# Kernel tuning notes

Measured on AMD Instinct MI355X. Metric: run time of the kernel, lower is better.

## Reference

```python
import jax, jax.numpy as jnp
import numpy as np
import math

HIDDEN = 1024
HEADS = 16
HEAD_DIM = HIDDEN // HEADS
B, S = 2, 2048


def setup_inputs() -> dict:
    key = jax.random.key(0)
    ks = jax.random.split(key, 10)
    std = 1.0 / math.sqrt(HIDDEN)
    mk = lambda k: (jax.random.normal(k, (HIDDEN, HIDDEN), jnp.float32) * std)
    return {
        "hidden_states": jax.random.normal(ks[0], (B, S, HIDDEN), jnp.float32),
        "attention_mask": jnp.zeros((B, 1, 1, S), jnp.float32),
        "wq": mk(ks[1]), "bq": jnp.zeros((HIDDEN,), jnp.float32),
        "wk": mk(ks[2]), "bk": jnp.zeros((HIDDEN,), jnp.float32),
        "wv": mk(ks[3]), "bv": jnp.zeros((HIDDEN,), jnp.float32),
        "wo": mk(ks[4]), "bo": jnp.zeros((HIDDEN,), jnp.float32),
    }


def reference(hidden_states, attention_mask, wq, bq, wk, bk, wv, bv, wo, bo):
    b, s, _ = hidden_states.shape
    scale = math.sqrt(HEAD_DIM)
    # projections (torch Linear: x @ W.T + b); weights stored as [out, in]
    q = hidden_states @ wq.T + bq
    k = hidden_states @ wk.T + bk
    v = hidden_states @ wv.T + bv
    # [B, H, S, D]
    q = q.reshape(b, s, HEADS, HEAD_DIM).transpose(0, 2, 1, 3)
    k = k.reshape(b, s, HEADS, HEAD_DIM).transpose(0, 2, 1, 3)
    v = v.reshape(b, s, HEADS, HEAD_DIM).transpose(0, 2, 1, 3)
    scores = jnp.einsum("bhqd,bhkd->bhqk", q, k) / scale
    scores = scores + attention_mask  # broadcast [B,1,1,S]
    weights = jax.nn.softmax(scores, axis=-1)  # dropout = identity (eval)
    out = jnp.einsum("bhqk,bhkd->bhqd", weights, v)
    out = out.transpose(0, 2, 1, 3).reshape(b, s, HIDDEN)
    out = out @ wo.T + bo
    return out
```

## Files before the change

kernel.cpp:

```cpp
#include <hip/hip_runtime.h>
#include <hip/hip_bf16.h>

typedef __bf16 bf16_t;
typedef __bf16 bf16x8 __attribute__((ext_vector_type(8)));
typedef float f32x4 __attribute__((ext_vector_type(4)));

#define SEQ    2048
#define NH     16
#define HD     64
#define HIDDEN 1024
#define PSTR   72
#define LOG2E  1.44269504f

__device__ __forceinline__ bf16_t to_bf16(float f) { return (bf16_t)f; }

__device__ __forceinline__ void async16(const bf16_t* g, bf16_t* l) {
    __builtin_amdgcn_global_load_lds((const __attribute__((address_space(1))) void*)g,
                                     (__attribute__((address_space(3))) void*)l, 16, 0, 0);
}

__global__ __launch_bounds__(256) void cvt_kernel(
    const float* __restrict__ s0, bf16_t* __restrict__ d0, int c0,
    const float* __restrict__ s1, bf16_t* __restrict__ d1, int c1,
    const float* __restrict__ s2, bf16_t* __restrict__ d2, int c2,
    const float* __restrict__ s3, bf16_t* __restrict__ d3, int c3)
{
    int blk = blockIdx.x;
    const float* s; bf16_t* d;
    if (blk < c0)              { s = s0; d = d0; }
    else if ((blk -= c0) < c1) { s = s1; d = d1; }
    else if ((blk -= c1) < c2) { s = s2; d = d2; }
    else                       { blk -= c2; s = s3; d = d3; }
    const size_t base = (size_t)blk * 2048 + threadIdx.x * 8;
    const float4 a = *(const float4*)&s[base];
    const float4 b = *(const float4*)&s[base + 4];
    bf16x8 o;
    o[0] = (bf16_t)a.x; o[1] = (bf16_t)a.y; o[2] = (bf16_t)a.z; o[3] = (bf16_t)a.w;
    o[4] = (bf16_t)b.x; o[5] = (bf16_t)b.y; o[6] = (bf16_t)b.z; o[7] = (bf16_t)b.w;
    *(bf16x8*)&d[base] = o;
}

__global__ __launch_bounds__(256, 3) void qkv_kernel(
    const bf16_t* __restrict__ X,
    const bf16_t* __restrict__ wq, const bf16_t* __restrict__ wk, const bf16_t* __restrict__ wv,
    const float* __restrict__ bq, const float* __restrict__ bk, const float* __restrict__ bv,
    bf16_t* __restrict__ qws, bf16_t* __restrict__ kws, bf16_t* __restrict__ vws)
{
    __shared__ __align__(16) bf16_t As[128 * 64];
    __shared__ __align__(16) bf16_t Bs[128 * 64];
    const int z = blockIdx.z;
    const bf16_t* Wsel = (z == 0) ? wq : (z == 1) ? wk : wv;
    const float*  bsel = (z == 0) ? bq : (z == 1) ? bk : bv;
    bf16_t* dst        = (z == 0) ? qws : (z == 1) ? kws : vws;
    const int m0 = blockIdx.y * 128, n0 = blockIdx.x * 128;

    const int t = threadIdx.x, lane = t & 63, w = t >> 6;
    const int w0 = w & 1, w1 = w >> 1, l15 = lane & 15, q4 = lane >> 4;

    f32x4 acc[4][4];
#pragma unroll
    for (int i = 0; i < 4; i++)
#pragma unroll
        for (int j = 0; j < 4; j++) acc[i][j] = f32x4{0.f, 0.f, 0.f, 0.f};

    for (int kt = 0; kt < HIDDEN; kt += 64) {
#pragma unroll
        for (int j = 0; j < 4; j++) {
            const int s = j * 256 + t;
            const int row = s >> 3, c = (s & 7) ^ (row & 7);
            const int lbase = (j * 256 + w * 64) * 8;
            async16(&X[(size_t)(m0 + row) * HIDDEN + kt + c * 8], &As[lbase]);
            async16(&Wsel[(size_t)(n0 + row) * HIDDEN + kt + c * 8], &Bs[lbase]);
        }
        __syncthreads();
#pragma unroll
        for (int ks = 0; ks < 2; ks++) {
            bf16x8 af[4];
#pragma unroll
            for (int ti = 0; ti < 4; ti++) {
                const int ra = w0 * 64 + ti * 16 + l15;
                af[ti] = *(const bf16x8*)&As[ra * 64 + (((ks * 4 + q4) ^ (ra & 7))) * 8];
            }
#pragma unroll
            for (int tj = 0; tj < 4; tj++) {
                const int rb = w1 * 64 + tj * 16 + l15;
                const bf16x8 bfr = *(const bf16x8*)&Bs[rb * 64 + (((ks * 4 + q4) ^ (rb & 7))) * 8];
#pragma unroll
                for (int ti = 0; ti < 4; ti++)
                    acc[ti][tj] = __builtin_amdgcn_mfma_f32_16x16x32_bf16(af[ti], bfr, acc[ti][tj], 0, 0, 0);
            }
        }
        __syncthreads();
    }

#pragma unroll
    for (int tj = 0; tj < 4; tj++) {
        const int n = n0 + w1 * 64 + tj * 16 + l15;
        const float bb = bsel[n];
        const int hh = n >> 6, d = n & 63;
#pragma unroll
        for (int ti = 0; ti < 4; ti++)
#pragma unroll
            for (int r = 0; r < 4; r++) {
                const int m = m0 + w0 * 64 + ti * 16 + q4 * 4 + r;
                const float val = acc[ti][tj][r] + bb;
                if (z < 2) {
                    dst[(size_t)m * HIDDEN + n] = to_bf16(val);
                } else {
                    const int b = m >> 11, s = m & (SEQ - 1);
                    dst[(((size_t)b * NH + hh) * HD + d) * SEQ + s] = to_bf16(val);
                }
            }
    }
}

__global__ __launch_bounds__(256, 2) void attn_kernel(
    const bf16_t* __restrict__ Qw, const bf16_t* __restrict__ Kw,
    const bf16_t* __restrict__ Vtw, const float* __restrict__ Mask,
    bf16_t* __restrict__ Ow)
{
    __shared__ __align__(16) bf16_t Ks[64 * 64];
    __shared__ __align__(16) bf16_t Vs[64 * 64];
    __shared__ __align__(16) bf16_t Ps[4 * 32 * PSTR];

    const int t = threadIdx.x, lane = t & 63, w = t >> 6;
    const int l15 = lane & 15, q4 = lane >> 4;
    const int lid = blockIdx.x + 16 * blockIdx.y;
    const int c8 = lid & 7, j = lid >> 3;
    const int bh = (c8 << 2) | (j >> 4);
    const int q0 = (j & 15) << 7;
    const int b = bh >> 4, h = bh & 15;

    const bf16_t* Qh = Qw + (size_t)b * SEQ * HIDDEN + h * HD;
    const bf16_t* Kh = Kw + (size_t)b * SEQ * HIDDEN + h * HD;
    const bf16_t* Vh = Vtw + (size_t)bh * HD * SEQ;
    const float* Mrow = Mask + (size_t)b * SEQ;

    bf16x8 qf[2][2];
#pragma unroll
    for (int rb = 0; rb < 2; rb++)
#pragma unroll
        for (int ks = 0; ks < 2; ks++)
            qf[rb][ks] = *(const bf16x8*)&Qh[(size_t)(q0 + w * 32 + rb * 16 + l15) * HIDDEN + ks * 32 + q4 * 8];

    f32x4 oacc[2][4];
#pragma unroll
    for (int rb = 0; rb < 2; rb++)
#pragma unroll
        for (int nb = 0; nb < 4; nb++) oacc[rb][nb] = f32x4{0.f, 0.f, 0.f, 0.f};
    float psum[2][4] = {{0.f, 0.f, 0.f, 0.f}, {0.f, 0.f, 0.f, 0.f}};

    for (int kt = 0; kt < SEQ; kt += 64) {
#pragma unroll
        for (int jj = 0; jj < 2; jj++) {
            const int s = jj * 256 + t;
            const int row = s >> 3, c = (s & 7) ^ (row & 7);
            const int lbase = (jj * 256 + w * 64) * 8;
            async16(&Kh[(size_t)(kt + row) * HIDDEN + c * 8], &Ks[lbase]);
            async16(&Vh[(size_t)row * SEQ + kt + c * 8], &Vs[lbase]);
        }
        __syncthreads();

        f32x4 sa[2][4];
#pragma unroll
        for (int rb = 0; rb < 2; rb++)
#pragma unroll
            for (int cb = 0; cb < 4; cb++) sa[rb][cb] = f32x4{0.f, 0.f, 0.f, 0.f};
#pragma unroll
        for (int cb = 0; cb < 4; cb++)
#pragma unroll
            for (int ks = 0; ks < 2; ks++) {
                const int r = cb * 16 + l15;
                const bf16x8 kf = *(const bf16x8*)&Ks[r * 64 + (((ks * 4 + q4) ^ (r & 7))) * 8];
                sa[0][cb] = __builtin_amdgcn_mfma_f32_16x16x32_bf16(qf[0][ks], kf, sa[0][cb], 0, 0, 0);
                sa[1][cb] = __builtin_amdgcn_mfma_f32_16x16x32_bf16(qf[1][ks], kf, sa[1][cb], 0, 0, 0);
            }

#pragma unroll
        for (int cb = 0; cb < 4; cb++) {
            const float mk2 = Mrow[kt + cb * 16 + l15] * LOG2E;
#pragma unroll
            for (int rb = 0; rb < 2; rb++)
#pragma unroll
                for (int r = 0; r < 4; r++) {
                    const float p = exp2f(fmaf(sa[rb][cb][r], 0.125f * LOG2E, mk2));
                    psum[rb][r] += p;
                    Ps[(w * 32 + rb * 16 + q4 * 4 + r) * PSTR + cb * 16 + l15] = to_bf16(p);
                }
        }

#pragma unroll
        for (int ks = 0; ks < 2; ks++) {
            const bf16x8 pf0 = *(const bf16x8*)&Ps[(w * 32 +      l15) * PSTR + ks * 32 + q4 * 8];
            const bf16x8 pf1 = *(const bf16x8*)&Ps[(w * 32 + 16 + l15) * PSTR + ks * 32 + q4 * 8];
#pragma unroll
            for (int nb = 0; nb < 4; nb++) {
                const int rv = nb * 16 + l15;
                const bf16x8 vf = *(const bf16x8*)&Vs[rv * 64 + (((ks * 4 + q4) ^ (rv & 7))) * 8];
                oacc[0][nb] = __builtin_amdgcn_mfma_f32_16x16x32_bf16(pf0, vf, oacc[0][nb], 0, 0, 0);
                oacc[1][nb] = __builtin_amdgcn_mfma_f32_16x16x32_bf16(pf1, vf, oacc[1][nb], 0, 0, 0);
            }
        }
        __syncthreads();
    }

#pragma unroll
    for (int rb = 0; rb < 2; rb++)
#pragma unroll
        for (int r = 0; r < 4; r++) {
#pragma unroll
            for (int off = 1; off < 16; off <<= 1) psum[rb][r] += __shfl_xor(psum[rb][r], off);
        }
#pragma unroll
    for (int rb = 0; rb < 2; rb++)
#pragma unroll
        for (int r = 0; r < 4; r++) {
            const float inv = 1.f / psum[rb][r];
            const int s = q0 + w * 32 + rb * 16 + q4 * 4 + r;
#pragma unroll
            for (int nb = 0; nb < 4; nb++) {
                const int d = nb * 16 + l15;
                Ow[((size_t)b * SEQ + s) * HIDDEN + h * HD + d] = to_bf16(oacc[rb][nb][r] * inv);
            }
        }
}

__global__ __launch_bounds__(256, 2) void oproj_kernel(
    const bf16_t* __restrict__ A, const bf16_t* __restrict__ Wo,
    const float* __restrict__ bo, float* __restrict__ Out)
{
    __shared__ __align__(16) bf16_t As[64 * 64];
    __shared__ __align__(16) bf16_t Bs[128 * 64];
    const int m0 = blockIdx.y * 64, n0 = blockIdx.x * 128;
    const int t = threadIdx.x, lane = t & 63, w = t >> 6;
    const int l15 = lane & 15, q4 = lane >> 4;

    f32x4 acc[4][2];
#pragma unroll
    for (int i = 0; i < 4; i++)
#pragma unroll
        for (int j = 0; j < 2; j++) acc[i][j] = f32x4{0.f, 0.f, 0.f, 0.f};

    for (int kt = 0; kt < HIDDEN; kt += 64) {
#pragma unroll
        for (int j = 0; j < 2; j++) {
            const int s = j * 256 + t;
            const int row = s >> 3, c = (s & 7) ^ (row & 7);
            async16(&A[(size_t)(m0 + row) * HIDDEN + kt + c * 8], &As[(j * 256 + w * 64) * 8]);
        }
#pragma unroll
        for (int j = 0; j < 4; j++) {
            const int s = j * 256 + t;
            const int row = s >> 3, c = (s & 7) ^ (row & 7);
            async16(&Wo[(size_t)(n0 + row) * HIDDEN + kt + c * 8], &Bs[(j * 256 + w * 64) * 8]);
        }
        __syncthreads();
#pragma unroll
        for (int ks = 0; ks < 2; ks++) {
            bf16x8 af[4];
#pragma unroll
            for (int ti = 0; ti < 4; ti++) {
                const int ra = ti * 16 + l15;
                af[ti] = *(const bf16x8*)&As[ra * 64 + (((ks * 4 + q4) ^ (ra & 7))) * 8];
            }
#pragma unroll
            for (int tj = 0; tj < 2; tj++) {
                const int rb = w * 32 + tj * 16 + l15;
                const bf16x8 bfr = *(const bf16x8*)&Bs[rb * 64 + (((ks * 4 + q4) ^ (rb & 7))) * 8];
#pragma unroll
                for (int ti = 0; ti < 4; ti++)
                    acc[ti][tj] = __builtin_amdgcn_mfma_f32_16x16x32_bf16(af[ti], bfr, acc[ti][tj], 0, 0, 0);
            }
        }
        __syncthreads();
    }

#pragma unroll
    for (int tj = 0; tj < 2; tj++) {
        const int n = n0 + w * 32 + tj * 16 + l15;
        const float bb = bo[n];
#pragma unroll
        for (int ti = 0; ti < 4; ti++)
#pragma unroll
            for (int r = 0; r < 4; r++) {
                const int m = m0 + ti * 16 + q4 * 4 + r;
                Out[(size_t)m * HIDDEN + n] = acc[ti][tj][r] + bb;
            }
    }
}

extern "C" void kernel_launch(void* const* d_in, const int* in_sizes, int n_in,
                              void* d_out, int out_size, void* d_ws, size_t ws_size,
                              hipStream_t stream) {
    const float* X   = (const float*)d_in[0];
    const float* msk = (const float*)d_in[1];
    const float* wq  = (const float*)d_in[2];
    const float* bq  = (const float*)d_in[3];
    const float* wk  = (const float*)d_in[4];
    const float* bk  = (const float*)d_in[5];
    const float* wv  = (const float*)d_in[6];
    const float* bv  = (const float*)d_in[7];
    const float* wo  = (const float*)d_in[8];
    const float* bo  = (const float*)d_in[9];
    float* out = (float*)d_out;

    const size_t NELT = (size_t)2 * SEQ * HIDDEN;
    const size_t WELT = (size_t)HIDDEN * HIDDEN;
    bf16_t* xbf = (bf16_t*)d_ws;
    bf16_t* qws = xbf + NELT;
    bf16_t* kws = qws + NELT;
    bf16_t* vws = kws + NELT;
    bf16_t* aws = xbf;
    bf16_t* wqb = (bf16_t*)d_out;
    bf16_t* wkb = wqb + WELT;
    bf16_t* wvb = wkb + WELT;
    bf16_t* wob = qws;

    cvt_kernel<<<dim3(2048 + 3 * 512), dim3(256), 0, stream>>>(
        X, xbf, 2048, wq, wqb, 512, wk, wkb, 512, wv, wvb, 512);
    qkv_kernel<<<dim3(8, 32, 3), dim3(256), 0, stream>>>(
        xbf, wqb, wkb, wvb, bq, bk, bv, qws, kws, vws);
    attn_kernel<<<dim3(16, 32), dim3(256), 0, stream>>>(qws, kws, vws, msk, aws);
    cvt_kernel<<<dim3(512), dim3(256), 0, stream>>>(
        wo, wob, 512, wo, wob, 0, wo, wob, 0, wo, wob, 0);
    oproj_kernel<<<dim3(8, 64), dim3(256), 0, stream>>>(aws, wob, bo, out);
}
```

Baseline: 229.5 us.

## Keep P in registers via transposed QK MFMA and split keys across warps

The attention kernel computes S^T (K as the A operand) so each lane already holds P in the layout needed for the PV MFMA. P is fed straight from registers as fp16 into 16x16x16 f16 MFMAs, which removes the shared-memory round trip for P. To support this, V is stored as fp16. Query tiles shrink to 64 rows, and the two warp pairs each process half of the key sequence. Their partial outputs and row sums are combined through LDS at the end. This doubles the grid to 1024 blocks and raises the occupancy hint to 4, at the cost of an extra reduction step and fp16 range limits on unnormalized probabilities.

```diff
diff --git a/kernel.cpp b/kernel.cpp
--- a/kernel.cpp
+++ b/kernel.cpp
@@ -3,18 +3,18 @@
 
 typedef __bf16 bf16_t;
 typedef __bf16 bf16x8 __attribute__((ext_vector_type(8)));
+typedef _Float16 f16x4 __attribute__((ext_vector_type(4)));
 typedef float f32x4 __attribute__((ext_vector_type(4)));
 
 #define SEQ    2048
 #define NH     16
 #define HD     64
 #define HIDDEN 1024
-#define PSTR   72
 #define LOG2E  1.44269504f
 
 __device__ __forceinline__ bf16_t to_bf16(float f) { return (bf16_t)f; }
 
-__device__ __forceinline__ void async16(const bf16_t* g, bf16_t* l) {
+__device__ __forceinline__ void async16(const void* g, void* l) {
     __builtin_amdgcn_global_load_lds((const __attribute__((address_space(1))) void*)g,
                                      (__attribute__((address_space(3))) void*)l, 16, 0, 0);
 }
@@ -44,14 +44,13 @@
     const bf16_t* __restrict__ X,
     const bf16_t* __restrict__ wq, const bf16_t* __restrict__ wk, const bf16_t* __restrict__ wv,
     const float* __restrict__ bq, const float* __restrict__ bk, const float* __restrict__ bv,
-    bf16_t* __restrict__ qws, bf16_t* __restrict__ kws, bf16_t* __restrict__ vws)
+    bf16_t* __restrict__ qws, bf16_t* __restrict__ kws, _Float16* __restrict__ vws)
 {
     __shared__ __align__(16) bf16_t As[128 * 64];
     __shared__ __align__(16) bf16_t Bs[128 * 64];
     const int z = blockIdx.z;
     const bf16_t* Wsel = (z == 0) ? wq : (z == 1) ? wk : wv;
     const float*  bsel = (z == 0) ? bq : (z == 1) ? bk : bv;
-    bf16_t* dst        = (z == 0) ? qws : (z == 1) ? kws : vws;
     const int m0 = blockIdx.y * 128, n0 = blockIdx.x * 128;
 
     const int t = threadIdx.x, lane = t & 63, w = t >> 6;
@@ -104,125 +103,153 @@
             for (int r = 0; r < 4; r++) {
                 const int m = m0 + w0 * 64 + ti * 16 + q4 * 4 + r;
                 const float val = acc[ti][tj][r] + bb;
-                if (z < 2) {
-                    dst[(size_t)m * HIDDEN + n] = to_bf16(val);
-                } else {
+                if (z == 0)      qws[(size_t)m * HIDDEN + n] = to_bf16(val);
+                else if (z == 1) kws[(size_t)m * HIDDEN + n] = to_bf16(val);
+                else {
                     const int b = m >> 11, s = m & (SEQ - 1);
-                    dst[(((size_t)b * NH + hh) * HD + d) * SEQ + s] = to_bf16(val);
+                    vws[(((size_t)b * NH + hh) * HD + d) * SEQ + s] = (_Float16)val;
                 }
             }
     }
 }
 
-__global__ __launch_bounds__(256, 2) void attn_kernel(
+__global__ __launch_bounds__(256, 4) void attn_kernel(
     const bf16_t* __restrict__ Qw, const bf16_t* __restrict__ Kw,
-    const bf16_t* __restrict__ Vtw, const float* __restrict__ Mask,
+    const _Float16* __restrict__ Vtw, const float* __restrict__ Mask,
     bf16_t* __restrict__ Ow)
 {
-    __shared__ __align__(16) bf16_t Ks[64 * 64];
-    __shared__ __align__(16) bf16_t Vs[64 * 64];
-    __shared__ __align__(16) bf16_t Ps[4 * 32 * PSTR];
+    __shared__ __align__(16) bf16_t Tiles[2][2][64 * 64];
 
     const int t = threadIdx.x, lane = t & 63, w = t >> 6;
     const int l15 = lane & 15, q4 = lane >> 4;
-    const int lid = blockIdx.x + 16 * blockIdx.y;
+    const int wq = w & 1, kh = w >> 1;
+    const int lid = blockIdx.x;
     const int c8 = lid & 7, j = lid >> 3;
-    const int bh = (c8 << 2) | (j >> 4);
-    const int q0 = (j & 15) << 7;
+    const int bh = c8 * 4 + (j >> 5);
+    const int q0 = (j & 31) * 64;
     const int b = bh >> 4, h = bh & 15;
 
     const bf16_t* Qh = Qw + (size_t)b * SEQ * HIDDEN + h * HD;
     const bf16_t* Kh = Kw + (size_t)b * SEQ * HIDDEN + h * HD;
-    const bf16_t* Vh = Vtw + (size_t)bh * HD * SEQ;
+    const _Float16* Vh = Vtw + (size_t)bh * HD * SEQ;
     const float* Mrow = Mask + (size_t)b * SEQ;
 
     bf16x8 qf[2][2];
 #pragma unroll
-    for (int rb = 0; rb < 2; rb++)
+    for (int nq = 0; nq < 2; nq++)
 #pragma unroll
         for (int ks = 0; ks < 2; ks++)
-            qf[rb][ks] = *(const bf16x8*)&Qh[(size_t)(q0 + w * 32 + rb * 16 + l15) * HIDDEN + ks * 32 + q4 * 8];
+            qf[nq][ks] = *(const bf16x8*)&Qh[(size_t)(q0 + wq * 32 + nq * 16 + l15) * HIDDEN + ks * 32 + q4 * 8];
 
     f32x4 oacc[2][4];
 #pragma unroll
-    for (int rb = 0; rb < 2; rb++)
-#pragma unroll
-        for (int nb = 0; nb < 4; nb++) oacc[rb][nb] = f32x4{0.f, 0.f, 0.f, 0.f};
-    float psum[2][4] = {{0.f, 0.f, 0.f, 0.f}, {0.f, 0.f, 0.f, 0.f}};
-
-    for (int kt = 0; kt < SEQ; kt += 64) {
-#pragma unroll
-        for (int jj = 0; jj < 2; jj++) {
-            const int s = jj * 256 + t;
+    for (int nq = 0; nq < 2; nq++)
+#pragma unroll
+        for (int nb = 0; nb < 4; nb++) oacc[nq][nb] = f32x4{0.f, 0.f, 0.f, 0.f};
+    float psum[2] = {0.f, 0.f};
+
+    bf16_t* Ksh = &Tiles[kh][0][0];
+    _Float16* Vsh = (_Float16*)&Tiles[kh][1][0];
+    const int kbase = kh * (SEQ / 2);
+
+    for (int it = 0; it < 16; it++) {
+        const int kt = kbase + it * 64;
+#pragma unroll
+        for (int jj = 0; jj < 4; jj++) {
+            const int s = jj * 128 + wq * 64 + lane;
             const int row = s >> 3, c = (s & 7) ^ (row & 7);
-            const int lbase = (jj * 256 + w * 64) * 8;
-            async16(&Kh[(size_t)(kt + row) * HIDDEN + c * 8], &Ks[lbase]);
-            async16(&Vh[(size_t)row * SEQ + kt + c * 8], &Vs[lbase]);
+            const int lbase = (jj * 128 + wq * 64) * 8;
+            async16(&Kh[(size_t)(kt + row) * HIDDEN + c * 8], &Ksh[lbase]);
+            async16(&Vh[(size_t)row * SEQ + kt + c * 8], &Vsh[lbase]);
         }
         __syncthreads();
 
         f32x4 sa[2][4];
 #pragma unroll
-        for (int rb = 0; rb < 2; rb++)
-#pragma unroll
-            for (int cb = 0; cb < 4; cb++) sa[rb][cb] = f32x4{0.f, 0.f, 0.f, 0.f};
+        for (int nq = 0; nq < 2; nq++)
+#pragma unroll
+            for (int cb = 0; cb < 4; cb++) sa[nq][cb] = f32x4{0.f, 0.f, 0.f, 0.f};
 #pragma unroll
         for (int cb = 0; cb < 4; cb++)
 #pragma unroll
             for (int ks = 0; ks < 2; ks++) {
-                const int r = cb * 16 + l15;
-                const bf16x8 kf = *(const bf16x8*)&Ks[r * 64 + (((ks * 4 + q4) ^ (r & 7))) * 8];
-                sa[0][cb] = __builtin_amdgcn_mfma_f32_16x16x32_bf16(qf[0][ks], kf, sa[0][cb], 0, 0, 0);
-                sa[1][cb] = __builtin_amdgcn_mfma_f32_16x16x32_bf16(qf[1][ks], kf, sa[1][cb], 0, 0, 0);
-            }
-
+                const int rk = cb * 16 + l15;
+                const bf16x8 kf = *(const bf16x8*)&Ksh[rk * 64 + (((ks * 4 + q4) ^ (rk & 7))) * 8];
+                sa[0][cb] = __builtin_amdgcn_mfma_f32_16x16x32_bf16(kf, qf[0][ks], sa[0][cb], 0, 0, 0);
+                sa[1][cb] = __builtin_amdgcn_mfma_f32_16x16x32_bf16(kf, qf[1][ks], sa[1][cb], 0, 0, 0);
+            }
+
+        f16x4 ph[2][4];
 #pragma unroll
         for (int cb = 0; cb < 4; cb++) {
-            const float mk2 = Mrow[kt + cb * 16 + l15] * LOG2E;
-#pragma unroll
-            for (int rb = 0; rb < 2; rb++)
+            float4 mv = *(const float4*)&Mrow[kt + cb * 16 + q4 * 4];
+            mv.x *= LOG2E; mv.y *= LOG2E; mv.z *= LOG2E; mv.w *= LOG2E;
+            const float mk[4] = {mv.x, mv.y, mv.z, mv.w};
+#pragma unroll
+            for (int nq = 0; nq < 2; nq++)
 #pragma unroll
                 for (int r = 0; r < 4; r++) {
-                    const float p = exp2f(fmaf(sa[rb][cb][r], 0.125f * LOG2E, mk2));
-                    psum[rb][r] += p;
-                    Ps[(w * 32 + rb * 16 + q4 * 4 + r) * PSTR + cb * 16 + l15] = to_bf16(p);
+                    const float p = exp2f(fmaf(sa[nq][cb][r], 0.125f * LOG2E, mk[r]));
+                    psum[nq] += p;
+                    ph[nq][cb][r] = (_Float16)p;
                 }
         }
 
 #pragma unroll
-        for (int ks = 0; ks < 2; ks++) {
-            const bf16x8 pf0 = *(const bf16x8*)&Ps[(w * 32 +      l15) * PSTR + ks * 32 + q4 * 8];
-            const bf16x8 pf1 = *(const bf16x8*)&Ps[(w * 32 + 16 + l15) * PSTR + ks * 32 + q4 * 8];
+        for (int cb = 0; cb < 4; cb++)
 #pragma unroll
             for (int nb = 0; nb < 4; nb++) {
                 const int rv = nb * 16 + l15;
-                const bf16x8 vf = *(const bf16x8*)&Vs[rv * 64 + (((ks * 4 + q4) ^ (rv & 7))) * 8];
-                oacc[0][nb] = __builtin_amdgcn_mfma_f32_16x16x32_bf16(pf0, vf, oacc[0][nb], 0, 0, 0);
-                oacc[1][nb] = __builtin_amdgcn_mfma_f32_16x16x32_bf16(pf1, vf, oacc[1][nb], 0, 0, 0);
-            }
-        }
-        __syncthreads();
-    }
-
-#pragma unroll
-    for (int rb = 0; rb < 2; rb++)
-#pragma unroll
-        for (int r = 0; r < 4; r++) {
-#pragma unroll
-            for (int off = 1; off < 16; off <<= 1) psum[rb][r] += __shfl_xor(psum[rb][r], off);
-        }
-#pragma unroll
-    for (int rb = 0; rb < 2; rb++)
-#pragma unroll
-        for (int r = 0; r < 4; r++) {
-            const float inv = 1.f / psum[rb][r];
-            const int s = q0 + w * 32 + rb * 16 + q4 * 4 + r;
+                const int cl = (cb * 2 + (q4 >> 1)) ^ (rv & 7);
+                const f16x4 vf = *(const f16x4*)&Vsh[rv * 64 + cl * 8 + (q4 & 1) * 4];
+                oacc[0][nb] = __builtin_amdgcn_mfma_f32_16x16x16f16(ph[0][cb], vf, oacc[0][nb], 0, 0, 0);
+                oacc[1][nb] = __builtin_amdgcn_mfma_f32_16x16x16f16(ph[1][cb], vf, oacc[1][nb], 0, 0, 0);
+            }
+        __syncthreads();
+    }
+
+#pragma unroll
+    for (int nq = 0; nq < 2; nq++) {
+        psum[nq] += __shfl_xor(psum[nq], 16);
+        psum[nq] += __shfl_xor(psum[nq], 32);
+    }
+
+    float* Cb = (float*)&Tiles[0][0][0];
+    if (kh == 1) {
+#pragma unroll
+        for (int nq = 0; nq < 2; nq++)
+#pragma unroll
+            for (int nb = 0; nb < 4; nb++)
+                *(f32x4*)&Cb[((size_t)(wq * 64 + lane)) * 32 + nq * 16 + nb * 4] = oacc[nq][nb];
+        Cb[4096 + wq * 128 + 0 * 64 + lane] = psum[0];
+        Cb[4096 + wq * 128 + 1 * 64 + lane] = psum[1];
+    }
+    __syncthreads();
+    if (kh == 0) {
+#pragma unroll
+        for (int nq = 0; nq < 2; nq++) {
 #pragma unroll
             for (int nb = 0; nb < 4; nb++) {
-                const int d = nb * 16 + l15;
-                Ow[((size_t)b * SEQ + s) * HIDDEN + h * HD + d] = to_bf16(oacc[rb][nb][r] * inv);
-            }
-        }
+                const f32x4 po = *(const f32x4*)&Cb[((size_t)(wq * 64 + lane)) * 32 + nq * 16 + nb * 4];
+                oacc[nq][nb] += po;
+            }
+            psum[nq] += Cb[4096 + wq * 128 + nq * 64 + lane];
+        }
+#pragma unroll
+        for (int nq = 0; nq < 2; nq++) {
+            float inv[4];
+#pragma unroll
+            for (int r = 0; r < 4; r++) inv[r] = 1.f / __shfl(psum[nq], q4 * 4 + r);
+#pragma unroll
+            for (int r = 0; r < 4; r++) {
+                const int s = q0 + wq * 32 + nq * 16 + q4 * 4 + r;
+#pragma unroll
+                for (int nb = 0; nb < 4; nb++)
+                    Ow[((size_t)b * SEQ + s) * HIDDEN + h * HD + nb * 16 + l15] =
+                        to_bf16(oacc[nq][nb][r] * inv[r]);
+            }
+        }
+    }
 }
 
 __global__ __launch_bounds__(256, 2) void oproj_kernel(
@@ -306,21 +333,21 @@
 
     const size_t NELT = (size_t)2 * SEQ * HIDDEN;
     const size_t WELT = (size_t)HIDDEN * HIDDEN;
-    bf16_t* xbf = (bf16_t*)d_ws;
-    bf16_t* qws = xbf + NELT;
-    bf16_t* kws = qws + NELT;
-    bf16_t* vws = kws + NELT;
-    bf16_t* aws = xbf;
-    bf16_t* wqb = (bf16_t*)d_out;
-    bf16_t* wkb = wqb + WELT;
-    bf16_t* wvb = wkb + WELT;
-    bf16_t* wob = qws;
+    bf16_t*    xbf = (bf16_t*)d_ws;
+    bf16_t*    qws = xbf + NELT;
+    bf16_t*    kws = qws + NELT;
+    _Float16*  vws = (_Float16*)(kws + NELT);
+    bf16_t*    aws = xbf;
+    bf16_t*    wqb = (bf16_t*)d_out;
+    bf16_t*    wkb = wqb + WELT;
+    bf16_t*    wvb = wkb + WELT;
+    bf16_t*    wob = qws;
 
     cvt_kernel<<<dim3(2048 + 3 * 512), dim3(256), 0, stream>>>(
         X, xbf, 2048, wq, wqb, 512, wk, wkb, 512, wv, wvb, 512);
     qkv_kernel<<<dim3(8, 32, 3), dim3(256), 0, stream>>>(
         xbf, wqb, wkb, wvb, bq, bk, bv, qws, kws, vws);
-    attn_kernel<<<dim3(16, 32), dim3(256), 0, stream>>>(qws, kws, vws, msk, aws);
+    attn_kernel<<<dim3(1024), dim3(256), 0, stream>>>(qws, kws, vws, msk, aws);
     cvt_kernel<<<dim3(512), dim3(256), 0, stream>>>(
         wo, wob, 512, wo, wob, 0, wo, wob, 0, wo, wob, 0);
     oproj_kernel<<<dim3(8, 64), dim3(256), 0, stream>>>(aws, wob, bo, out);
```

Result: faster. 214.7 us (-6.4%).
